# Performance work log

Hardware: AMD Instinct MI355X
Metric: run time of the kernel (lower is better)

## Reference

```python
import jax, jax.numpy as jnp
import numpy as np

N, C, H, W = 16, 128, 48, 48
CI = C // 2  # inter_channels


def setup_inputs() -> dict:
    key = jax.random.key(0)
    ks = jax.random.split(key, 9)
    s_in = 1.0 / np.sqrt(C)
    s_out = 1.0 / np.sqrt(CI)
    return {
        "features": jax.random.normal(ks[0], (N, C, H, W), jnp.float32),
        "Wq": jax.random.normal(ks[1], (CI, C), jnp.float32) * s_in,
        "bq": jax.random.normal(ks[2], (CI,), jnp.float32) * 0.01,
        "Wk": jax.random.normal(ks[3], (CI, C), jnp.float32) * s_in,
        "bk": jax.random.normal(ks[4], (CI,), jnp.float32) * 0.01,
        "Wv": jax.random.normal(ks[5], (CI, C), jnp.float32) * s_in,
        "bv": jax.random.normal(ks[6], (CI,), jnp.float32) * 0.01,
        "Wz": jax.random.normal(ks[7], (C, CI), jnp.float32) * s_out,
        "bz": jax.random.normal(ks[8], (C,), jnp.float32) * 0.01,
    }


def reference(features, Wq, bq, Wk, bk, Wv, bv, Wz, bz):
    n, c, h, w = features.shape
    hw = h * w

    def proj(x, Wp, bp):
        # conv1x1 over (n, c, h, w) -> tokens (n, hw, ci)
        t = jnp.einsum('nchw,dc->ndhw', x, Wp) + bp[None, :, None, None]
        return t.reshape(n, -1, hw).transpose(0, 2, 1)

    q = proj(features, Wq, bq)   # (n, hw, ci)
    k = proj(features, Wk, bk)
    v = proj(features, Wv, bv)

    # before/after neighbor slices with edge clamping (slice 0 / slice n-1 use themselves)
    kb = jnp.concatenate([k[:1], k[:-1]], axis=0)
    vb = jnp.concatenate([v[:1], v[:-1]], axis=0)
    ka = jnp.concatenate([k[1:], k[-1:]], axis=0)
    va = jnp.concatenate([v[1:], v[-1:]], axis=0)

    def attend(kk, vv):
        f = jnp.einsum('nqd,nkd->nqk', q, kk)        # (n, hw, hw); no 1/sqrt(d) scale, per original
        a = jax.nn.softmax(f, axis=-1)
        y = jnp.einsum('nqk,nkd->nqd', a, vv)        # (n, hw, ci)
        z = jnp.einsum('nqd,cd->nqc', y, Wz) + bz    # W_z conv1x1
        return z.transpose(0, 2, 1).reshape(n, c, h, w)

    return attend(kb, vb) + attend(ka, va) + features
```

## Files before the change

kernel.cpp:

```cpp
#include <hip/hip_runtime.h>
#include <math.h>

#define NBATCH 16
#define CCH    128
#define HW     2304
#define DI     64
#define NTILE  36

typedef unsigned short u16;
typedef unsigned int   u32;
typedef __bf16   bf16x8 __attribute__((ext_vector_type(8)));
typedef _Float16 f16x8  __attribute__((ext_vector_type(8)));
typedef float    f32x4  __attribute__((ext_vector_type(4)));

__device__ __forceinline__ u16 f2bf_rne(float x) {
    union { float f; u32 u; } v; v.f = x;
    u32 r = (v.u + 0x7FFFu + ((v.u >> 16) & 1u)) >> 16;
    return (u16)r;
}
__device__ __forceinline__ u16 f2h(float x) {
    union { _Float16 h; u16 u; } c; c.h = (_Float16)x; return c.u;
}

__global__ __launch_bounds__(256) void wprep_kernel(
    const float* __restrict__ Wq, const float* __restrict__ Wk,
    const float* __restrict__ Wv, const float* __restrict__ Wz,
    u16* __restrict__ Wf, u16* __restrict__ Wzf)
{
    const int idx  = blockIdx.x * 256 + threadIdx.x;
    if (idx < 3072) {
        const int lane = idx & 63;
        const int fi   = idx >> 6;
        const int g = fi >> 2, ks = fi & 3;
        const int lo = lane & 15, hi = lane >> 4;
        const int row = g * 16 + lo;
        const float* src = (row < 64)  ? &Wq[row * CCH]
                         : (row < 128) ? &Wk[(row - 64) * CCH]
                                       : &Wv[(row - 128) * CCH];
        const int c0 = (ks * 4 + hi) * 8;
        float4 a = *(const float4*)&src[c0];
        float4 b = *(const float4*)&src[c0 + 4];
        union { u16 s8[8]; uint4 v; } pk;
        pk.s8[0] = f2h(a.x); pk.s8[1] = f2h(a.y); pk.s8[2] = f2h(a.z); pk.s8[3] = f2h(a.w);
        pk.s8[4] = f2h(b.x); pk.s8[5] = f2h(b.y); pk.s8[6] = f2h(b.z); pk.s8[7] = f2h(b.w);
        *(uint4*)&Wf[(size_t)idx * 8] = pk.v;
    } else {
        const int t    = idx - 3072;
        const int lane = t & 63;
        const int fi   = t >> 6;
        const int g = fi >> 1, ks = fi & 1;
        const int lo = lane & 15, hi = lane >> 4;
        const int row = g * 16 + lo;
        const int d0  = ks * 32 + hi * 8;
        float4 a = *(const float4*)&Wz[row * DI + d0];
        float4 b = *(const float4*)&Wz[row * DI + d0 + 4];
        union { u16 s8[8]; uint4 v; } pk;
        pk.s8[0] = f2h(a.x); pk.s8[1] = f2h(a.y); pk.s8[2] = f2h(a.z); pk.s8[3] = f2h(a.w);
        pk.s8[4] = f2h(b.x); pk.s8[5] = f2h(b.y); pk.s8[6] = f2h(b.z); pk.s8[7] = f2h(b.w);
        *(uint4*)&Wzf[(size_t)t * 8] = pk.v;
    }
}

__global__ __launch_bounds__(256) void proj_kernel(
    const float* __restrict__ F, const u16* __restrict__ Wf,
    const float* __restrict__ bq, const float* __restrict__ bk,
    const float* __restrict__ bv,
    u16* __restrict__ qo, u16* __restrict__ ko, u16* __restrict__ vto)
{
    __shared__ __align__(16) u16 Fl[64 * 128];
    __shared__ __align__(16) u16 Vt[64 * 72];

    const int tid  = threadIdx.x;
    const int n    = blockIdx.x / NTILE;
    const int p0   = (blockIdx.x % NTILE) * 64;
    const int lane = tid & 63, wave = tid >> 6;
    const int lo   = lane & 15, hi = lane >> 4;

    const float* Fn = F + (size_t)n * CCH * HW;
    #pragma unroll
    for (int i = 0; i < 4; ++i) {
        int s  = tid + i * 256;
        int c0 = (s >> 4) * 2;
        int t0 = (s & 15) * 4;
        const float* fp_ = &Fn[(size_t)c0 * HW + p0 + t0];
        float4 fa = *(const float4*)fp_;
        float4 fb = *(const float4*)(fp_ + HW);
        #pragma unroll
        for (int e = 0; e < 4; ++e) {
            int t = t0 + e;
            u32 w = (u32)f2h((&fa.x)[e]) | ((u32)f2h((&fb.x)[e]) << 16);
            *(u32*)&Fl[t * 128 + (((c0 >> 3) ^ (t & 15)) << 3) + (c0 & 7)] = w;
        }
    }
    __syncthreads();

    const int arow = wave * 16 + lo;
    f16x8 af[4];
    #pragma unroll
    for (int ks = 0; ks < 4; ++ks)
        af[ks] = *(const f16x8*)&Fl[arow * 128 + (((ks * 4 + hi) ^ lo) << 3)];

    f32x4 acc[12];
    #pragma unroll
    for (int g = 0; g < 12; ++g)
        #pragma unroll
        for (int r = 0; r < 4; ++r) acc[g][r] = 0.f;

    #pragma unroll
    for (int g = 0; g < 12; ++g) {
        #pragma unroll
        for (int ks = 0; ks < 4; ++ks) {
            f16x8 bf = *(const f16x8*)&Wf[(size_t)((g * 4 + ks) * 64 + lane) * 8];
            acc[g] = __builtin_amdgcn_mfma_f32_16x16x32_f16(af[ks], bf, acc[g], 0, 0, 0);
        }
    }

    const int twb = p0 + wave * 16 + 4 * hi;
    #pragma unroll
    for (int g = 0; g < 4; ++g) {
        float bQ = bq[g * 16 + lo], bK = bk[g * 16 + lo];
        #pragma unroll
        for (int r = 0; r < 4; ++r) {
            size_t off = ((size_t)n * HW + twb + r) * DI + g * 16 + lo;
            qo[off] = f2h(acc[g][r] + bQ);
            ko[off] = f2h(acc[g + 4][r] + bK);
        }
    }
    #pragma unroll
    for (int g = 0; g < 4; ++g) {
        float bV = bv[g * 16 + lo];
        #pragma unroll
        for (int r = 0; r < 4; ++r)
            Vt[(g * 16 + lo) * 72 + wave * 16 + 4 * hi + r] = f2bf_rne(acc[g + 8][r] + bV);
    }
    __syncthreads();
    #pragma unroll
    for (int i = 0; i < 2; ++i) {
        int s = tid + i * 256;
        int d = s >> 3, c8 = (s & 7) * 8;
        *(uint4*)&vto[((size_t)n * DI + d) * HW + p0 + c8] = *(const uint4*)&Vt[d * 72 + c8];
    }
}

__global__ __launch_bounds__(256, 4) void attn_pass_kernel(
    const u16* __restrict__ q, const u16* __restrict__ k, const u16* __restrict__ vt,
    u16* __restrict__ ypart)
{
    __shared__ __align__(16) u16 smem[16384];
    u16* const Kb0 = smem;
    u16* const Kb1 = smem + 4096;
    u16* const Vb0 = smem + 8192;
    u16* const Vb1 = smem + 12288;

    const int tid  = threadIdx.x;
    const int lane = tid & 63;
    const int wave = tid >> 6;
    const int lo   = lane & 15, hi = lane >> 4;

    const int bid  = (int)blockIdx.x;
    const int w    = (bid & 7) * 144 + (bid >> 3);
    const int pass = w / (NBATCH * NTILE);
    const int rem  = w % (NBATCH * NTILE);
    const int n    = rem / NTILE;
    const int p0   = (rem % NTILE) * 64;

    const int nb = (pass == 0) ? (n > 0 ? n - 1 : 0)
                               : (n < NBATCH - 1 ? n + 1 : n);
    const u16* kp = k  + (size_t)nb * HW * DI;
    const u16* vp = vt + (size_t)nb * DI * HW;

    f16x8 qf0, qf1;
    {
        const u16* qp = q + ((size_t)n * HW + p0 + wave * 16 + lo) * DI + hi * 8;
        qf0 = *(const f16x8*)qp;
        qf1 = *(const f16x8*)(qp + 32);
    }

    const int sch   = tid & 7;
    const int srow0 = tid >> 3;
    const int srow1 = srow0 + 32;
    const int fk0   = (srow0 & 3) | ((srow0 & 8) >> 1);
    const int fk1   = (srow1 & 3) | ((srow1 & 8) >> 1);
    const int koff0 = srow0 * 64 + ((sch ^ fk0) * 8);
    const int koff1 = srow1 * 64 + ((sch ^ fk1) * 8);
    const int voff0 = srow0 * 64 + ((sch ^ (srow0 & 7)) * 8);
    const int voff1 = srow1 * 64 + ((sch ^ (srow1 & 7)) * 8);

    const int krbase = 8 * (lo >> 2) + (lo & 3);
    const int xl = lo & 7;

    f32x4 yacc[4];
    #pragma unroll
    for (int nf = 0; nf < 4; ++nf)
        #pragma unroll
        for (int r = 0; r < 4; ++r) yacc[nf][r] = 0.f;
    float lacc = 0.f;

    uint4 ka0 = *(const uint4*)(kp + (size_t)srow0 * DI + sch * 8);
    uint4 ka1 = *(const uint4*)(kp + (size_t)srow1 * DI + sch * 8);
    uint4 va0 = *(const uint4*)(vp + (size_t)srow0 * HW + sch * 8);
    uint4 va1 = *(const uint4*)(vp + (size_t)srow1 * HW + sch * 8);
    *(uint4*)&Kb0[koff0] = ka0;  *(uint4*)&Kb0[koff1] = ka1;
    *(uint4*)&Vb0[voff0] = va0;  *(uint4*)&Vb0[voff1] = va1;
    ka0 = *(const uint4*)(kp + (size_t)(64 + srow0) * DI + sch * 8);
    ka1 = *(const uint4*)(kp + (size_t)(64 + srow1) * DI + sch * 8);
    va0 = *(const uint4*)(vp + (size_t)srow0 * HW + 64 + sch * 8);
    va1 = *(const uint4*)(vp + (size_t)srow1 * HW + 64 + sch * 8);
    __syncthreads();

    auto body = [&](int t, const u16* Kc, const u16* Vc, u16* Kn, u16* Vn) {
        f32x4 st[4];
        __builtin_amdgcn_s_setprio(1);
        #pragma unroll
        for (int m = 0; m < 4; ++m) {
            const int kr = krbase + 4 * (m & 1) + 32 * (m >> 1);
            f16x8 a0 = *(const f16x8*)&Kc[kr * 64 + ((hi ^ xl) * 8)];
            f16x8 a1 = *(const f16x8*)&Kc[kr * 64 + (((4 + hi) ^ xl) * 8)];
            f32x4 z = {0.f, 0.f, 0.f, 0.f};
            z = __builtin_amdgcn_mfma_f32_16x16x32_f16(a0, qf0, z, 0, 0, 0);
            z = __builtin_amdgcn_mfma_f32_16x16x32_f16(a1, qf1, z, 0, 0, 0);
            st[m] = z;
        }
        __builtin_amdgcn_s_setprio(0);

        bf16x8 pa0, pa1;
        #pragma unroll
        for (int m = 0; m < 4; ++m) {
            float e0 = __expf(st[m][0]);
            float e1 = __expf(st[m][1]);
            float e2 = __expf(st[m][2]);
            float e3 = __expf(st[m][3]);
            lacc += (e0 + e1) + (e2 + e3);
            __bf16 b0 = (__bf16)e0, b1 = (__bf16)e1, b2 = (__bf16)e2, b3 = (__bf16)e3;
            if (m == 0)      { pa0[0] = b0; pa0[1] = b1; pa0[2] = b2; pa0[3] = b3; }
            else if (m == 1) { pa0[4] = b0; pa0[5] = b1; pa0[6] = b2; pa0[7] = b3; }
            else if (m == 2) { pa1[0] = b0; pa1[1] = b1; pa1[2] = b2; pa1[3] = b3; }
            else             { pa1[4] = b0; pa1[5] = b1; pa1[6] = b2; pa1[7] = b3; }
        }

        __builtin_amdgcn_s_setprio(1);
        #pragma unroll
        for (int nf = 0; nf < 4; ++nf) {
            const int vr = nf * 16 + lo;
            bf16x8 v0 = *(const bf16x8*)&Vc[vr * 64 + ((hi ^ xl) * 8)];
            bf16x8 v1 = *(const bf16x8*)&Vc[vr * 64 + (((4 + hi) ^ xl) * 8)];
            yacc[nf] = __builtin_amdgcn_mfma_f32_16x16x32_bf16(pa0, v0, yacc[nf], 0, 0, 0);
            yacc[nf] = __builtin_amdgcn_mfma_f32_16x16x32_bf16(pa1, v1, yacc[nf], 0, 0, 0);
        }
        __builtin_amdgcn_s_setprio(0);

        if (t + 1 < NTILE) {
            *(uint4*)&Kn[koff0] = ka0; *(uint4*)&Kn[koff1] = ka1;
            *(uint4*)&Vn[voff0] = va0; *(uint4*)&Vn[voff1] = va1;
        }
        if (t + 2 < NTILE) {
            int tb = (t + 2) * 64;
            ka0 = *(const uint4*)(kp + (size_t)(tb + srow0) * DI + sch * 8);
            ka1 = *(const uint4*)(kp + (size_t)(tb + srow1) * DI + sch * 8);
            va0 = *(const uint4*)(vp + (size_t)srow0 * HW + tb + sch * 8);
            va1 = *(const uint4*)(vp + (size_t)srow1 * HW + tb + sch * 8);
        }
        __syncthreads();
    };

    #pragma unroll 1
    for (int tt = 0; tt < NTILE; tt += 2) {
        body(tt,     Kb0, Vb0, Kb1, Vb1);
        body(tt + 1, Kb1, Vb1, Kb0, Vb0);
    }

    float l = lacc;
    l += __shfl_xor(l, 16);
    l += __shfl_xor(l, 32);
    float inv = 1.f / l;
    float invq[4];
    #pragma unroll
    for (int r = 0; r < 4; ++r) invq[r] = __shfl(inv, 20 * hi + r);

    __syncthreads();
    u16* yw = smem;
    #pragma unroll
    for (int nf = 0; nf < 4; ++nf)
        #pragma unroll
        for (int r = 0; r < 4; ++r)
            yw[(wave * 16 + hi * 4 + r) * 72 + nf * 16 + lo] =
                f2h(yacc[nf][r] * invq[r]);
    __syncthreads();

    u16* yg = ypart + ((size_t)(pass * NBATCH + n) * HW + p0) * DI;
    #pragma unroll
    for (int s = 0; s < 2; ++s) {
        int idx = tid + s * 256;
        int row = idx >> 3, c8 = (idx & 7) * 8;
        *(uint4*)&yg[row * DI + c8] = *(const uint4*)&yw[row * 72 + c8];
    }
}

__global__ __launch_bounds__(256) void combine_kernel(
    const u16* __restrict__ ypart, const u16* __restrict__ Wzf,
    const float* __restrict__ bz, const float* __restrict__ F,
    float* __restrict__ out)
{
    __shared__ __align__(16) float zs[64 * 129];
    const int tid  = threadIdx.x;
    const int n    = blockIdx.x / NTILE;
    const int p0   = (blockIdx.x % NTILE) * 64;
    const int lane = tid & 63, wave = tid >> 6;
    const int lo   = lane & 15, hi = lane >> 4;

    const u16* y0 = ypart + ((size_t)n * HW + p0 + wave * 16 + lo) * DI;
    const u16* y1 = ypart + ((size_t)(NBATCH + n) * HW + p0 + wave * 16 + lo) * DI;
    f16x8 a00 = *(const f16x8*)(y0 + hi * 8);
    f16x8 a01 = *(const f16x8*)(y0 + 32 + hi * 8);
    f16x8 a10 = *(const f16x8*)(y1 + hi * 8);
    f16x8 a11 = *(const f16x8*)(y1 + 32 + hi * 8);

    f32x4 acc[8];
    #pragma unroll
    for (int g = 0; g < 8; ++g)
        #pragma unroll
        for (int r = 0; r < 4; ++r) acc[g][r] = 0.f;

    #pragma unroll
    for (int g = 0; g < 8; ++g) {
        f16x8 b0 = *(const f16x8*)&Wzf[(size_t)((g * 2 + 0) * 64 + lane) * 8];
        f16x8 b1 = *(const f16x8*)&Wzf[(size_t)((g * 2 + 1) * 64 + lane) * 8];
        acc[g] = __builtin_amdgcn_mfma_f32_16x16x32_f16(a00, b0, acc[g], 0, 0, 0);
        acc[g] = __builtin_amdgcn_mfma_f32_16x16x32_f16(a01, b1, acc[g], 0, 0, 0);
        acc[g] = __builtin_amdgcn_mfma_f32_16x16x32_f16(a10, b0, acc[g], 0, 0, 0);
        acc[g] = __builtin_amdgcn_mfma_f32_16x16x32_f16(a11, b1, acc[g], 0, 0, 0);
    }

    #pragma unroll
    for (int g = 0; g < 8; ++g)
        #pragma unroll
        for (int r = 0; r < 4; ++r)
            zs[(wave * 16 + 4 * hi + r) * 129 + g * 16 + lo] = acc[g][r];
    __syncthreads();

    #pragma unroll 4
    for (int i = 0; i < 32; ++i) {
        int c = wave + 4 * i;
        size_t gi = (size_t)(n * CCH + c) * HW + p0 + lane;
        out[gi] = zs[lane * 129 + c] + 2.f * bz[c] + F[gi];
    }
}

extern "C" void kernel_launch(void* const* d_in, const int* in_sizes, int n_in,
                              void* d_out, int out_size, void* d_ws, size_t ws_size,
                              hipStream_t stream) {
    const float* F  = (const float*)d_in[0];
    const float* Wq = (const float*)d_in[1];
    const float* bq = (const float*)d_in[2];
    const float* Wk = (const float*)d_in[3];
    const float* bk = (const float*)d_in[4];
    const float* Wv = (const float*)d_in[5];
    const float* bv = (const float*)d_in[6];
    const float* Wz = (const float*)d_in[7];
    const float* bz = (const float*)d_in[8];
    float* outp = (float*)d_out;

    const size_t tok = (size_t)NBATCH * HW * DI;
    u16* qb  = (u16*)d_ws;
    u16* kb  = qb  + tok;
    u16* vtb = kb  + tok;
    u16* yp  = vtb + tok;
    u16* wf  = yp  + 2 * tok;
    u16* wzf = wf  + 24576;

    wprep_kernel<<<16, 256, 0, stream>>>(Wq, Wk, Wv, Wz, wf, wzf);
    proj_kernel<<<NBATCH * NTILE, 256, 0, stream>>>(F, wf, bq, bk, bv, qb, kb, vtb);
    attn_pass_kernel<<<2 * NBATCH * NTILE, 256, 0, stream>>>(qb, kb, vtb, yp);
    combine_kernel<<<NBATCH * NTILE, 256, 0, stream>>>(yp, wzf, bz, F, outp);
}
```

Before: 97.61 us.

## Split key range across two half-blocks and widen query tile to 128 rows

The attention kernel now uses 512-thread blocks covering 128 query rows. Each wave handles two 16-row query fragments, so every K/V fragment read from LDS feeds twice as many MFMAs. The key range is split between two groups of four waves, each with its own double-buffered K/V staging. Their partial softmax sums and outputs are merged through shared memory in fp16 at the end. This halves the block count, doubles LDS per block, and adds a cross-half reduction step and extra register pressure.

```diff
diff --git a/kernel.cpp b/kernel.cpp
--- a/kernel.cpp
+++ b/kernel.cpp
@@ -6,6 +6,8 @@
 #define HW     2304
 #define DI     64
 #define NTILE  36
+#define HTILE  18
+#define QBLK   18
 
 typedef unsigned short u16;
 typedef unsigned int   u32;
@@ -21,6 +23,11 @@
 __device__ __forceinline__ u16 f2h(float x) {
     union { _Float16 h; u16 u; } c; c.h = (_Float16)x; return c.u;
 }
+__device__ __forceinline__ u32 pkh(float a, float b) {
+    union { _Float16 h[2]; u32 u; } c; c.h[0] = (_Float16)a; c.h[1] = (_Float16)b; return c.u;
+}
+__device__ __forceinline__ float h0f(u32 w) { union { u32 u; _Float16 h[2]; } c; c.u = w; return (float)c.h[0]; }
+__device__ __forceinline__ float h1f(u32 w) { union { u32 u; _Float16 h[2]; } c; c.u = w; return (float)c.h[1]; }
 
 __global__ __launch_bounds__(256) void wprep_kernel(
     const float* __restrict__ Wq, const float* __restrict__ Wk,
@@ -142,42 +149,48 @@
     }
 }
 
-__global__ __launch_bounds__(256, 4) void attn_pass_kernel(
+__global__ __launch_bounds__(512, 4) void attn_pass_kernel(
     const u16* __restrict__ q, const u16* __restrict__ k, const u16* __restrict__ vt,
     u16* __restrict__ ypart)
 {
-    __shared__ __align__(16) u16 smem[16384];
-    u16* const Kb0 = smem;
-    u16* const Kb1 = smem + 4096;
-    u16* const Vb0 = smem + 8192;
-    u16* const Vb1 = smem + 12288;
-
+    __shared__ __align__(16) u16 smem[32768];
     const int tid  = threadIdx.x;
     const int lane = tid & 63;
     const int wave = tid >> 6;
+    const int w4   = wave & 3;
+    const int half = wave >> 2;
     const int lo   = lane & 15, hi = lane >> 4;
 
     const int bid  = (int)blockIdx.x;
-    const int w    = (bid & 7) * 144 + (bid >> 3);
-    const int pass = w / (NBATCH * NTILE);
-    const int rem  = w % (NBATCH * NTILE);
-    const int n    = rem / NTILE;
-    const int p0   = (rem % NTILE) * 64;
+    const int w    = (bid & 7) * 72 + (bid >> 3);
+    const int pass = w / (NBATCH * QBLK);
+    const int rem  = w % (NBATCH * QBLK);
+    const int n    = rem / QBLK;
+    const int p0   = (rem % QBLK) * 128;
 
     const int nb = (pass == 0) ? (n > 0 ? n - 1 : 0)
                                : (n < NBATCH - 1 ? n + 1 : n);
     const u16* kp = k  + (size_t)nb * HW * DI;
     const u16* vp = vt + (size_t)nb * DI * HW;
-
-    f16x8 qf0, qf1;
+    const int  kq = half * (HTILE * 64);
+
+    u16* const Kb0 = smem + half * 8192;
+    u16* const Kb1 = Kb0 + 4096;
+    u16* const Vb0 = smem + 16384 + half * 8192;
+    u16* const Vb1 = Vb0 + 4096;
+
+    f16x8 qfA0, qfA1, qfB0, qfB1;
     {
-        const u16* qp = q + ((size_t)n * HW + p0 + wave * 16 + lo) * DI + hi * 8;
-        qf0 = *(const f16x8*)qp;
-        qf1 = *(const f16x8*)(qp + 32);
-    }
-
-    const int sch   = tid & 7;
-    const int srow0 = tid >> 3;
+        const u16* qp = q + ((size_t)n * HW + p0 + w4 * 32 + lo) * DI + hi * 8;
+        qfA0 = *(const f16x8*)qp;
+        qfA1 = *(const f16x8*)(qp + 32);
+        qfB0 = *(const f16x8*)(qp + 16 * DI);
+        qfB1 = *(const f16x8*)(qp + 16 * DI + 32);
+    }
+
+    const int stid  = tid & 255;
+    const int sch   = stid & 7;
+    const int srow0 = stid >> 3;
     const int srow1 = srow0 + 32;
     const int fk0   = (srow0 & 3) | ((srow0 & 8) >> 1);
     const int fk1   = (srow1 & 3) | ((srow1 & 8) >> 1);
@@ -189,53 +202,70 @@
     const int krbase = 8 * (lo >> 2) + (lo & 3);
     const int xl = lo & 7;
 
-    f32x4 yacc[4];
+    f32x4 yaccA[4], yaccB[4];
     #pragma unroll
     for (int nf = 0; nf < 4; ++nf)
         #pragma unroll
-        for (int r = 0; r < 4; ++r) yacc[nf][r] = 0.f;
-    float lacc = 0.f;
-
-    uint4 ka0 = *(const uint4*)(kp + (size_t)srow0 * DI + sch * 8);
-    uint4 ka1 = *(const uint4*)(kp + (size_t)srow1 * DI + sch * 8);
-    uint4 va0 = *(const uint4*)(vp + (size_t)srow0 * HW + sch * 8);
-    uint4 va1 = *(const uint4*)(vp + (size_t)srow1 * HW + sch * 8);
+        for (int r = 0; r < 4; ++r) { yaccA[nf][r] = 0.f; yaccB[nf][r] = 0.f; }
+    float laccA = 0.f, laccB = 0.f;
+
+    uint4 ka0 = *(const uint4*)(kp + (size_t)(kq + srow0) * DI + sch * 8);
+    uint4 ka1 = *(const uint4*)(kp + (size_t)(kq + srow1) * DI + sch * 8);
+    uint4 va0 = *(const uint4*)(vp + (size_t)srow0 * HW + kq + sch * 8);
+    uint4 va1 = *(const uint4*)(vp + (size_t)srow1 * HW + kq + sch * 8);
     *(uint4*)&Kb0[koff0] = ka0;  *(uint4*)&Kb0[koff1] = ka1;
     *(uint4*)&Vb0[voff0] = va0;  *(uint4*)&Vb0[voff1] = va1;
-    ka0 = *(const uint4*)(kp + (size_t)(64 + srow0) * DI + sch * 8);
-    ka1 = *(const uint4*)(kp + (size_t)(64 + srow1) * DI + sch * 8);
-    va0 = *(const uint4*)(vp + (size_t)srow0 * HW + 64 + sch * 8);
-    va1 = *(const uint4*)(vp + (size_t)srow1 * HW + 64 + sch * 8);
+    ka0 = *(const uint4*)(kp + (size_t)(kq + 64 + srow0) * DI + sch * 8);
+    ka1 = *(const uint4*)(kp + (size_t)(kq + 64 + srow1) * DI + sch * 8);
+    va0 = *(const uint4*)(vp + (size_t)srow0 * HW + kq + 64 + sch * 8);
+    va1 = *(const uint4*)(vp + (size_t)srow1 * HW + kq + 64 + sch * 8);
     __syncthreads();
 
     auto body = [&](int t, const u16* Kc, const u16* Vc, u16* Kn, u16* Vn) {
-        f32x4 st[4];
+        f32x4 stA[4], stB[4];
         __builtin_amdgcn_s_setprio(1);
         #pragma unroll
         for (int m = 0; m < 4; ++m) {
             const int kr = krbase + 4 * (m & 1) + 32 * (m >> 1);
             f16x8 a0 = *(const f16x8*)&Kc[kr * 64 + ((hi ^ xl) * 8)];
             f16x8 a1 = *(const f16x8*)&Kc[kr * 64 + (((4 + hi) ^ xl) * 8)];
-            f32x4 z = {0.f, 0.f, 0.f, 0.f};
-            z = __builtin_amdgcn_mfma_f32_16x16x32_f16(a0, qf0, z, 0, 0, 0);
-            z = __builtin_amdgcn_mfma_f32_16x16x32_f16(a1, qf1, z, 0, 0, 0);
-            st[m] = z;
+            f32x4 zA = {0.f, 0.f, 0.f, 0.f};
+            zA = __builtin_amdgcn_mfma_f32_16x16x32_f16(a0, qfA0, zA, 0, 0, 0);
+            zA = __builtin_amdgcn_mfma_f32_16x16x32_f16(a1, qfA1, zA, 0, 0, 0);
+            stA[m] = zA;
+            f32x4 zB = {0.f, 0.f, 0.f, 0.f};
+            zB = __builtin_amdgcn_mfma_f32_16x16x32_f16(a0, qfB0, zB, 0, 0, 0);
+            zB = __builtin_amdgcn_mfma_f32_16x16x32_f16(a1, qfB1, zB, 0, 0, 0);
+            stB[m] = zB;
         }
         __builtin_amdgcn_s_setprio(0);
 
-        bf16x8 pa0, pa1;
+        bf16x8 paA0, paA1, paB0, paB1;
         #pragma unroll
         for (int m = 0; m < 4; ++m) {
-            float e0 = __expf(st[m][0]);
-            float e1 = __expf(st[m][1]);
-            float e2 = __expf(st[m][2]);
-            float e3 = __expf(st[m][3]);
-            lacc += (e0 + e1) + (e2 + e3);
+            float e0 = __expf(stA[m][0]);
+            float e1 = __expf(stA[m][1]);
+            float e2 = __expf(stA[m][2]);
+            float e3 = __expf(stA[m][3]);
+            laccA += (e0 + e1) + (e2 + e3);
             __bf16 b0 = (__bf16)e0, b1 = (__bf16)e1, b2 = (__bf16)e2, b3 = (__bf16)e3;
-            if (m == 0)      { pa0[0] = b0; pa0[1] = b1; pa0[2] = b2; pa0[3] = b3; }
-            else if (m == 1) { pa0[4] = b0; pa0[5] = b1; pa0[6] = b2; pa0[7] = b3; }
-            else if (m == 2) { pa1[0] = b0; pa1[1] = b1; pa1[2] = b2; pa1[3] = b3; }
-            else             { pa1[4] = b0; pa1[5] = b1; pa1[6] = b2; pa1[7] = b3; }
+            if (m == 0)      { paA0[0] = b0; paA0[1] = b1; paA0[2] = b2; paA0[3] = b3; }
+            else if (m == 1) { paA0[4] = b0; paA0[5] = b1; paA0[6] = b2; paA0[7] = b3; }
+            else if (m == 2) { paA1[0] = b0; paA1[1] = b1; paA1[2] = b2; paA1[3] = b3; }
+            else             { paA1[4] = b0; paA1[5] = b1; paA1[6] = b2; paA1[7] = b3; }
+        }
+        #pragma unroll
+        for (int m = 0; m < 4; ++m) {
+            float e0 = __expf(stB[m][0]);
+            float e1 = __expf(stB[m][1]);
+            float e2 = __expf(stB[m][2]);
+            float e3 = __expf(stB[m][3]);
+            laccB += (e0 + e1) + (e2 + e3);
+            __bf16 b0 = (__bf16)e0, b1 = (__bf16)e1, b2 = (__bf16)e2, b3 = (__bf16)e3;
+            if (m == 0)      { paB0[0] = b0; paB0[1] = b1; paB0[2] = b2; paB0[3] = b3; }
+            else if (m == 1) { paB0[4] = b0; paB0[5] = b1; paB0[6] = b2; paB0[7] = b3; }
+            else if (m == 2) { paB1[0] = b0; paB1[1] = b1; paB1[2] = b2; paB1[3] = b3; }
+            else             { paB1[4] = b0; paB1[5] = b1; paB1[6] = b2; paB1[7] = b3; }
         }
 
         __builtin_amdgcn_s_setprio(1);
@@ -244,17 +274,19 @@
             const int vr = nf * 16 + lo;
             bf16x8 v0 = *(const bf16x8*)&Vc[vr * 64 + ((hi ^ xl) * 8)];
             bf16x8 v1 = *(const bf16x8*)&Vc[vr * 64 + (((4 + hi) ^ xl) * 8)];
-            yacc[nf] = __builtin_amdgcn_mfma_f32_16x16x32_bf16(pa0, v0, yacc[nf], 0, 0, 0);
-            yacc[nf] = __builtin_amdgcn_mfma_f32_16x16x32_bf16(pa1, v1, yacc[nf], 0, 0, 0);
+            yaccA[nf] = __builtin_amdgcn_mfma_f32_16x16x32_bf16(paA0, v0, yaccA[nf], 0, 0, 0);
+            yaccA[nf] = __builtin_amdgcn_mfma_f32_16x16x32_bf16(paA1, v1, yaccA[nf], 0, 0, 0);
+            yaccB[nf] = __builtin_amdgcn_mfma_f32_16x16x32_bf16(paB0, v0, yaccB[nf], 0, 0, 0);
+            yaccB[nf] = __builtin_amdgcn_mfma_f32_16x16x32_bf16(paB1, v1, yaccB[nf], 0, 0, 0);
         }
         __builtin_amdgcn_s_setprio(0);
 
-        if (t + 1 < NTILE) {
+        if (t + 1 < HTILE) {
             *(uint4*)&Kn[koff0] = ka0; *(uint4*)&Kn[koff1] = ka1;
             *(uint4*)&Vn[voff0] = va0; *(uint4*)&Vn[voff1] = va1;
         }
-        if (t + 2 < NTILE) {
-            int tb = (t + 2) * 64;
+        if (t + 2 < HTILE) {
+            int tb = kq + (t + 2) * 64;
             ka0 = *(const uint4*)(kp + (size_t)(tb + srow0) * DI + sch * 8);
             ka1 = *(const uint4*)(kp + (size_t)(tb + srow1) * DI + sch * 8);
             va0 = *(const uint4*)(vp + (size_t)srow0 * HW + tb + sch * 8);
@@ -264,33 +296,80 @@
     };
 
     #pragma unroll 1
-    for (int tt = 0; tt < NTILE; tt += 2) {
+    for (int tt = 0; tt < HTILE; tt += 2) {
         body(tt,     Kb0, Vb0, Kb1, Vb1);
         body(tt + 1, Kb1, Vb1, Kb0, Vb0);
     }
 
-    float l = lacc;
-    l += __shfl_xor(l, 16);
-    l += __shfl_xor(l, 32);
-    float inv = 1.f / l;
-    float invq[4];
-    #pragma unroll
-    for (int r = 0; r < 4; ++r) invq[r] = __shfl(inv, 20 * hi + r);
-
-    __syncthreads();
-    u16* yw = smem;
+    float lA = laccA;
+    lA += __shfl_xor(lA, 16);
+    lA += __shfl_xor(lA, 32);
+    float lB = laccB;
+    lB += __shfl_xor(lB, 16);
+    lB += __shfl_xor(lB, 32);
+
+    float* Ll = (float*)smem;
+    u32*   X  = (u32*)((char*)smem + 4096);
+    u16*   yw = smem + 10240;
+
+    if (hi == 0) {
+        Ll[((half * 4 + w4) * 2 + 0) * 16 + lo] = lA;
+        Ll[((half * 4 + w4) * 2 + 1) * 16 + lo] = lB;
+    }
+    __syncthreads();
+
+    float sA[4], sB[4];
+    #pragma unroll
+    for (int r = 0; r < 4; ++r) {
+        int qr = 4 * hi + r;
+        sA[r] = 1.f / (Ll[((0 * 4 + w4) * 2 + 0) * 16 + qr] + Ll[((1 * 4 + w4) * 2 + 0) * 16 + qr]);
+        sB[r] = 1.f / (Ll[((0 * 4 + w4) * 2 + 1) * 16 + qr] + Ll[((1 * 4 + w4) * 2 + 1) * 16 + qr]);
+    }
+    float zA[4][4], zB[4][4];
     #pragma unroll
     for (int nf = 0; nf < 4; ++nf)
         #pragma unroll
-        for (int r = 0; r < 4; ++r)
-            yw[(wave * 16 + hi * 4 + r) * 72 + nf * 16 + lo] =
-                f2h(yacc[nf][r] * invq[r]);
+        for (int r = 0; r < 4; ++r) {
+            zA[nf][r] = yaccA[nf][r] * sA[r];
+            zB[nf][r] = yaccB[nf][r] * sB[r];
+        }
+
+    u32* Xl = &X[(w4 * 64 + lane) * 16];
+    if (half == 1) {
+        #pragma unroll
+        for (int nf = 0; nf < 4; ++nf) {
+            Xl[nf * 2 + 0]     = pkh(zA[nf][0], zA[nf][1]);
+            Xl[nf * 2 + 1]     = pkh(zA[nf][2], zA[nf][3]);
+            Xl[8 + nf * 2 + 0] = pkh(zB[nf][0], zB[nf][1]);
+            Xl[8 + nf * 2 + 1] = pkh(zB[nf][2], zB[nf][3]);
+        }
+    }
+    __syncthreads();
+
+    if (half == 0) {
+        #pragma unroll
+        for (int nf = 0; nf < 4; ++nf) {
+            u32 wa0 = Xl[nf * 2 + 0], wa1 = Xl[nf * 2 + 1];
+            u32 wb0 = Xl[8 + nf * 2 + 0], wb1 = Xl[8 + nf * 2 + 1];
+            zA[nf][0] += h0f(wa0); zA[nf][1] += h1f(wa0);
+            zA[nf][2] += h0f(wa1); zA[nf][3] += h1f(wa1);
+            zB[nf][0] += h0f(wb0); zB[nf][1] += h1f(wb0);
+            zB[nf][2] += h0f(wb1); zB[nf][3] += h1f(wb1);
+        }
+        #pragma unroll
+        for (int nf = 0; nf < 4; ++nf)
+            #pragma unroll
+            for (int r = 0; r < 4; ++r) {
+                yw[(w4 * 32 + 4 * hi + r) * 72 + nf * 16 + lo]      = f2h(zA[nf][r]);
+                yw[(w4 * 32 + 16 + 4 * hi + r) * 72 + nf * 16 + lo] = f2h(zB[nf][r]);
+            }
+    }
     __syncthreads();
 
     u16* yg = ypart + ((size_t)(pass * NBATCH + n) * HW + p0) * DI;
     #pragma unroll
     for (int s = 0; s < 2; ++s) {
-        int idx = tid + s * 256;
+        int idx = tid + s * 512;
         int row = idx >> 3, c8 = (idx & 7) * 8;
         *(uint4*)&yg[row * DI + c8] = *(const uint4*)&yw[row * 72 + c8];
     }
@@ -307,9 +386,10 @@
     const int p0   = (blockIdx.x % NTILE) * 64;
     const int lane = tid & 63, wave = tid >> 6;
     const int lo   = lane & 15, hi = lane >> 4;
-
-    const u16* y0 = ypart + ((size_t)n * HW + p0 + wave * 16 + lo) * DI;
-    const u16* y1 = ypart + ((size_t)(NBATCH + n) * HW + p0 + wave * 16 + lo) * DI;
+    (void)lo;
+
+    const u16* y0 = ypart + ((size_t)n * HW + p0 + wave * 16 + (lane & 15)) * DI;
+    const u16* y1 = ypart + ((size_t)(NBATCH + n) * HW + p0 + wave * 16 + (lane & 15)) * DI;
     f16x8 a00 = *(const f16x8*)(y0 + hi * 8);
     f16x8 a01 = *(const f16x8*)(y0 + 32 + hi * 8);
     f16x8 a10 = *(const f16x8*)(y1 + hi * 8);
@@ -335,7 +415,7 @@
     for (int g = 0; g < 8; ++g)
         #pragma unroll
         for (int r = 0; r < 4; ++r)
-            zs[(wave * 16 + 4 * hi + r) * 129 + g * 16 + lo] = acc[g][r];
+            zs[(wave * 16 + 4 * hi + r) * 129 + g * 16 + (lane & 15)] = acc[g][r];
     __syncthreads();
 
     #pragma unroll 4
@@ -370,6 +450,6 @@
 
     wprep_kernel<<<16, 256, 0, stream>>>(Wq, Wk, Wv, Wz, wf, wzf);
     proj_kernel<<<NBATCH * NTILE, 256, 0, stream>>>(F, wf, bq, bk, bv, qb, kb, vtb);
-    attn_pass_kernel<<<2 * NBATCH * NTILE, 256, 0, stream>>>(qb, kb, vtb, yp);
+    attn_pass_kernel<<<2 * NBATCH * QBLK, 512, 0, stream>>>(qb, kb, vtb, yp);
     combine_kernel<<<NBATCH * NTILE, 256, 0, stream>>>(yp, wzf, bz, F, outp);
 }
```

Result: slower. 363.6 us (+272.5%).
